# Optimization experiments

Hardware: AMD Instinct MI355X
Metric: run time of the kernel (lower is better)

## Reference

```python
import jax, jax.numpy as jnp
import numpy as np

N = 50000
F_IN = 256
HID = 64
HEADS = 4
NUM_CLASSES = 40
E = 1600000
NEG_SLOPE = 0.2
BN_EPS = 1e-5


def setup_inputs() -> dict:
    key = jax.random.key(0)
    ks = jax.random.split(key, 16)
    x = jax.random.normal(ks[0], (N, F_IN), dtype=jnp.float32)
    edge_index = jax.random.randint(ks[1], (2, E), 0, N, dtype=jnp.int64)
    # layer 1: GATConv(F_IN -> HID, heads=HEADS), PyG param layout
    W1 = jax.random.normal(ks[2], (F_IN, HEADS * HID), dtype=jnp.float32) / np.sqrt(F_IN)
    att_src1 = jax.random.normal(ks[3], (HEADS, HID), dtype=jnp.float32) / np.sqrt(HID)
    att_dst1 = jax.random.normal(ks[4], (HEADS, HID), dtype=jnp.float32) / np.sqrt(HID)
    bias1 = jnp.zeros((HEADS * HID,), dtype=jnp.float32)
    # BatchNorm1d(HEADS*HID), eval mode running stats
    gamma1 = jax.random.normal(ks[5], (HEADS * HID,), dtype=jnp.float32) * 0.1 + 1.0
    beta1 = jax.random.normal(ks[6], (HEADS * HID,), dtype=jnp.float32) * 0.1
    mean1 = jax.random.normal(ks[7], (HEADS * HID,), dtype=jnp.float32) * 0.1
    var1 = jax.random.uniform(ks[8], (HEADS * HID,), dtype=jnp.float32) + 0.5
    # layer 2: GATConv(HEADS*HID -> NUM_CLASSES, heads=1)
    W2 = jax.random.normal(ks[9], (HEADS * HID, NUM_CLASSES), dtype=jnp.float32) / np.sqrt(HEADS * HID)
    att_src2 = jax.random.normal(ks[10], (1, NUM_CLASSES), dtype=jnp.float32) / np.sqrt(NUM_CLASSES)
    att_dst2 = jax.random.normal(ks[11], (1, NUM_CLASSES), dtype=jnp.float32) / np.sqrt(NUM_CLASSES)
    bias2 = jnp.zeros((NUM_CLASSES,), dtype=jnp.float32)
    return {
        "x": x, "edge_index": edge_index,
        "W1": W1, "att_src1": att_src1, "att_dst1": att_dst1, "bias1": bias1,
        "gamma1": gamma1, "beta1": beta1, "mean1": mean1, "var1": var1,
        "W2": W2, "att_src2": att_src2, "att_dst2": att_dst2, "bias2": bias2,
    }


def gat_conv(x, src, dst, W, att_src, att_dst, bias, heads, out_ch):
    n = x.shape[0]
    h = (x @ W).reshape(n, heads, out_ch)          # [N, H, C]
    a_src = jnp.sum(h * att_src, axis=-1)           # [N, H]
    a_dst = jnp.sum(h * att_dst, axis=-1)           # [N, H]
    e = jax.nn.leaky_relu(a_src[src] + a_dst[dst], NEG_SLOPE)  # [E, H]
    # softmax over incoming edges per destination node
    e_max = jax.ops.segment_max(e, dst, num_segments=n)        # [N, H]
    e = jnp.exp(e - e_max[dst])
    denom = jax.ops.segment_sum(e, dst, num_segments=n)        # [N, H]
    alpha = e / (denom[dst] + 1e-16)                # [E, H]
    msg = h[src] * alpha[:, :, None]                # [E, H, C]
    out = jax.ops.segment_sum(msg, dst, num_segments=n)        # [N, H, C]
    return out.reshape(n, heads * out_ch) + bias


def reference(x, edge_index, W1, att_src1, att_dst1, bias1,
              gamma1, beta1, mean1, var1,
              W2, att_src2, att_dst2, bias2):
    # add self loops (PyG GATConv default add_self_loops=True)
    loop = jnp.arange(N, dtype=edge_index.dtype)
    src = jnp.concatenate([edge_index[0], loop])
    dst = jnp.concatenate([edge_index[1], loop])
    h = gat_conv(x, src, dst, W1, att_src1, att_dst1, bias1, HEADS, HID)
    # BatchNorm1d eval mode + ELU (dropout inactive in eval)
    h = (h - mean1) * jax.lax.rsqrt(var1 + BN_EPS) * gamma1 + beta1
    h = jax.nn.elu(h)
    out = gat_conv(h, src, dst, W2, att_src2, att_dst2, bias2, 1, NUM_CLASSES)
    return out
```

## Files before the change

kernel.cpp:

```cpp
#include <hip/hip_runtime.h>
#include <hip/hip_bf16.h>

#define NN 50000
#define FIN 256
#define F1 256
#define HEADS 4
#define HID 64
#define NC 40
#define NE 1600000
#define SLOPE 0.2f
#define LOG2E 1.44269504f
#define CHUNK 128
#define NB2 98
#define BSH 9
#define BCAP2 18000
#define TILE 2048
#define NBIN 782
#define NG1 782
#define G1PAD 40

typedef unsigned int u32;
typedef unsigned short u16;
typedef unsigned char u8;
typedef __attribute__((ext_vector_type(8))) short bf16x8;
typedef __attribute__((ext_vector_type(4))) float f32x4;

__device__ __forceinline__ float us2f(u32 u){ u32 b = u << 16; return __uint_as_float(b); }
__device__ __forceinline__ u16 f2bf(float f){
  u32 b = __float_as_uint(f);
  u32 r = (b + 0x7fffu + ((b >> 16) & 1u)) >> 16;
  return (u16)r;
}

__global__ __launch_bounds__(256) void k_prep(const int* __restrict__ ei,
      int* __restrict__ cnt, u32* __restrict__ bin,
      const float* __restrict__ W1, u16* __restrict__ w1h, u16* __restrict__ w1l,
      const float* __restrict__ W2, u16* __restrict__ w2h, u16* __restrict__ w2l){
  __shared__ int hcnt[NB2], hoff[NB2], gbase[NB2], hcur[NB2];
  __shared__ u32 staged[TILE];
  __shared__ u8  sbk[TILE];
  __shared__ int ci;
  int bid = blockIdx.x, tid = threadIdx.x;
  if(bid < NBIN){
    int e0 = bid * TILE;
    int nn = min(TILE, NE - e0);
    if(tid==0) ci = 0;
    for(int b=tid;b<NB2;b+=256) hcnt[b] = 0;
    __syncthreads();
    if(ei[2*(e0+tid)+1] != 0) atomicAdd(&ci, 1);
    __syncthreads();
    int i64 = (ci == 0);
    u32 val[TILE/256]; int bk[TILE/256];
    #pragma unroll
    for(int j=0;j<TILE/256;j++){
      int t = tid + j*256;
      if(t < nn){
        int i = e0 + t;
        int src = i64 ? ei[2*i] : ei[i];
        int dst = i64 ? ei[2*(NE+i)] : ei[NE+i];
        bk[j] = dst >> BSH;
        val[j] = (u32)src | ((u32)(dst & 511) << 16);
        atomicAdd(&hcnt[bk[j]], 1);
      } else bk[j] = -1;
    }
    __syncthreads();
    if(tid == 0){
      int run = 0;
      for(int b=0;b<NB2;b++){ hoff[b] = run; hcur[b] = run; run += hcnt[b]; }
    }
    __syncthreads();
    if(tid < NB2 && hcnt[tid] > 0) gbase[tid] = atomicAdd(&cnt[tid], hcnt[tid]);
    __syncthreads();
    #pragma unroll
    for(int j=0;j<TILE/256;j++){
      if(bk[j] >= 0){
        int pos = atomicAdd(&hcur[bk[j]], 1);
        staged[pos] = val[j];
        sbk[pos] = (u8)bk[j];
      }
    }
    __syncthreads();
    for(int s=tid; s<nn; s+=256){
      int b = sbk[s];
      int local = gbase[b] + (s - hoff[b]);
      if(local < BCAP2) bin[(size_t)b*BCAP2 + local] = staged[s];
    }
  } else if(bid < NBIN+256){
    int id = (bid-NBIN)*256 + tid;
    int n = id & 255, k = id >> 8;
    float v = W1[k*F1 + n];
    u16 h = f2bf(v);
    w1h[n*FIN + k] = h;
    w1l[n*FIN + k] = f2bf(v - us2f(h));
  } else {
    int id = (bid-(NBIN+256))*256 + tid;
    int col = id >> 8, k = id & 255;
    float v = (col < NC) ? W2[k*NC + col] : 0.f;
    u16 h = f2bf(v);
    w2h[col*F1 + k] = h;
    w2l[col*F1 + k] = f2bf(v - us2f(h));
  }
}

__global__ __launch_bounds__(256) void k_g1h(const float* __restrict__ x,
                                             const short* __restrict__ wh, const short* __restrict__ wl,
                                             const float* __restrict__ as1, const float* __restrict__ ad1,
                                             u16* __restrict__ h1b,
                                             float* __restrict__ aS, float* __restrict__ aD,
                                             const int* __restrict__ cnt, const u32* __restrict__ bin,
                                             int* __restrict__ rloc, int* __restrict__ bsum){
  __shared__ char smem[4*128*G1PAD*2];
  int tid = threadIdx.x;
  if(blockIdx.x >= NG1){
    int* dl = (int*)smem; int* s1 = dl + 512; int* s2 = s1 + 512;
    int b = blockIdx.x - NG1;
    for(int i=tid;i<512;i+=256) dl[i] = 0;
    __syncthreads();
    int n = min(cnt[b], BCAP2);
    const u32* bp = bin + (size_t)b*BCAP2;
    for(int i=tid;i<n;i+=256) atomicAdd(&dl[(bp[i]>>16)&511], 1);
    __syncthreads();
    for(int i=tid;i<512;i+=256) s1[i] = dl[i];
    __syncthreads();
    int* src = s1; int* dst = s2;
    for(int off=1; off<512; off<<=1){
      for(int i=tid;i<512;i+=256) dst[i] = src[i] + (i>=off ? src[i-off] : 0);
      __syncthreads();
      int* t = src; src = dst; dst = t;
    }
    for(int i=tid;i<512;i+=256) rloc[b*512+i] = src[i] - dl[i];
    if(tid==0) bsum[b] = src[511];
    return;
  }
  u16* Ah = (u16*)smem;
  u16* Al = Ah + 128*G1PAD;
  u16* Bh = Al + 128*G1PAD;
  u16* Bl = Bh + 128*G1PAD;
  int w = tid >> 6, lane = tid & 63;
  int lo = lane & 15, hi = lane >> 4;
  int bidm = blockIdx.x >> 1, bidn = blockIdx.x & 1;
  int rowbase = bidm*128, colbase = bidn*128;
  int wr = w >> 1, wc = w & 1;
  int r0 = tid >> 2, ch = tid & 3;
  int arow0 = rowbase + r0;      if(arow0 >= NN) arow0 = NN-1;
  int arow1 = rowbase + r0 + 64; if(arow1 >= NN) arow1 = NN-1;
  const float* pX0 = x + (size_t)arow0*FIN + ch*8;
  const float* pX1 = x + (size_t)arow1*FIN + ch*8;
  const short* pB0h = wh + (size_t)(colbase + r0)*FIN + ch*8;
  const short* pB1h = wh + (size_t)(colbase + r0 + 64)*FIN + ch*8;
  const short* pB0l = wl + (size_t)(colbase + r0)*FIN + ch*8;
  const short* pB1l = wl + (size_t)(colbase + r0 + 64)*FIN + ch*8;
  int so0 = r0*G1PAD + ch*8, so1 = (r0+64)*G1PAD + ch*8;
  f32x4 acc[4][4];
  #pragma unroll
  for(int rg=0;rg<4;rg++)
    #pragma unroll
    for(int tt=0;tt<4;tt++) acc[rg][tt] = (f32x4){0.f,0.f,0.f,0.f};
  for(int k0=0; k0<FIN; k0+=32){
    float4 xa0 = *(const float4*)(pX0 + k0);
    float4 xa1 = *(const float4*)(pX0 + k0 + 4);
    float4 xb0 = *(const float4*)(pX1 + k0);
    float4 xb1 = *(const float4*)(pX1 + k0 + 4);
    bf16x8 vb0 = *(const bf16x8*)(pB0h + k0);
    bf16x8 vb1 = *(const bf16x8*)(pB1h + k0);
    bf16x8 vb2 = *(const bf16x8*)(pB0l + k0);
    bf16x8 vb3 = *(const bf16x8*)(pB1l + k0);
    float v0[8] = {xa0.x,xa0.y,xa0.z,xa0.w,xa1.x,xa1.y,xa1.z,xa1.w};
    float v1[8] = {xb0.x,xb0.y,xb0.z,xb0.w,xb1.x,xb1.y,xb1.z,xb1.w};
    bf16x8 a0h, a0l, a1h, a1l;
    #pragma unroll
    for(int j=0;j<8;j++){
      u32 u = __float_as_uint(v0[j]);
      a0h[j] = (short)(u >> 16);
      float hf = __uint_as_float(u & 0xffff0000u);
      a0l[j] = (short)(__float_as_uint(v0[j] - hf) >> 16);
      u32 u2 = __float_as_uint(v1[j]);
      a1h[j] = (short)(u2 >> 16);
      float hf2 = __uint_as_float(u2 & 0xffff0000u);
      a1l[j] = (short)(__float_as_uint(v1[j] - hf2) >> 16);
    }
    __syncthreads();
    *(bf16x8*)&Ah[so0] = a0h; *(bf16x8*)&Ah[so1] = a1h;
    *(bf16x8*)&Al[so0] = a0l; *(bf16x8*)&Al[so1] = a1l;
    *(bf16x8*)&Bh[so0] = vb0; *(bf16x8*)&Bh[so1] = vb1;
    *(bf16x8*)&Bl[so0] = vb2; *(bf16x8*)&Bl[so1] = vb3;
    __syncthreads();
    bf16x8 ah[4], al[4];
    #pragma unroll
    for(int rg=0;rg<4;rg++){
      int ar = wr*64 + rg*16 + lo;
      ah[rg] = *(const bf16x8*)&Ah[ar*G1PAD + hi*8];
      al[rg] = *(const bf16x8*)&Al[ar*G1PAD + hi*8];
    }
    #pragma unroll
    for(int tt=0;tt<4;tt++){
      int bc = wc*64 + tt*16 + lo;
      bf16x8 bh = *(const bf16x8*)&Bh[bc*G1PAD + hi*8];
      bf16x8 bl = *(const bf16x8*)&Bl[bc*G1PAD + hi*8];
      #pragma unroll
      for(int rg=0;rg<4;rg++){
        acc[rg][tt] = __builtin_amdgcn_mfma_f32_16x16x32_bf16(ah[rg], bh, acc[rg][tt], 0, 0, 0);
        acc[rg][tt] = __builtin_amdgcn_mfma_f32_16x16x32_bf16(al[rg], bh, acc[rg][tt], 0, 0, 0);
        acc[rg][tt] = __builtin_amdgcn_mfma_f32_16x16x32_bf16(ah[rg], bl, acc[rg][tt], 0, 0, 0);
      }
    }
  }
  #pragma unroll
  for(int rg=0;rg<4;rg++){
    #pragma unroll
    for(int tt=0;tt<4;tt++){
      #pragma unroll
      for(int r=0;r<4;r++){
        int row = rowbase + wr*64 + rg*16 + hi*4 + r;
        if(row < NN) h1b[(size_t)row*F1 + colbase + wc*64 + tt*16 + lo] = f2bf(acc[rg][tt][r]);
      }
    }
  }
  int head = bidn*2 + wc;
  float ps[4][4], pd[4][4];
  #pragma unroll
  for(int rg=0;rg<4;rg++)
    #pragma unroll
    for(int r=0;r<4;r++){ ps[rg][r]=0.f; pd[rg][r]=0.f; }
  #pragma unroll
  for(int tt=0;tt<4;tt++){
    int col = colbase + wc*64 + tt*16 + lo;
    float sv = as1[col]*LOG2E, dv = ad1[col]*LOG2E;
    #pragma unroll
    for(int rg=0;rg<4;rg++)
      #pragma unroll
      for(int r=0;r<4;r++){ ps[rg][r] += acc[rg][tt][r]*sv; pd[rg][r] += acc[rg][tt][r]*dv; }
  }
  #pragma unroll
  for(int off=1; off<16; off<<=1){
    #pragma unroll
    for(int rg=0;rg<4;rg++)
      #pragma unroll
      for(int r=0;r<4;r++){
        ps[rg][r] += __shfl_xor(ps[rg][r], off, 64);
        pd[rg][r] += __shfl_xor(pd[rg][r], off, 64);
      }
  }
  if(lo == 0){
    #pragma unroll
    for(int rg=0;rg<4;rg++)
      #pragma unroll
      for(int r=0;r<4;r++){
        int row = rowbase + wr*64 + rg*16 + hi*4 + r;
        if(row < NN){ aS[row*HEADS+head] = ps[rg][r]; aD[row*HEADS+head] = pd[rg][r]; }
      }
  }
}

__global__ __launch_bounds__(256) void k_fill2(const int* __restrict__ cnt, const u32* __restrict__ bin,
                                               const int* __restrict__ rloc, const int* __restrict__ bsum,
                                               int* __restrict__ rowptr, int* __restrict__ adj){
  __shared__ int cur[512];
  __shared__ int sb[NB2];
  __shared__ int base_s;
  int b = blockIdx.x, tid = threadIdx.x;
  if(tid < NB2) sb[tid] = bsum[tid];
  __syncthreads();
  if(tid == 0){
    int run = 0;
    for(int i=0;i<b;i++) run += sb[i];
    base_s = run;
    if(b == NB2-1) rowptr[NN] = run + sb[b];
  }
  __syncthreads();
  int base = base_s;
  for(int i=tid;i<512;i+=256){
    int d = b*512 + i;
    int v = base + rloc[b*512+i];
    cur[i] = v;
    if(d < NN) rowptr[d] = v;
  }
  __syncthreads();
  int n = min(cnt[b], BCAP2);
  const u32* bp = bin + (size_t)b*BCAP2;
  for(int i=tid;i<n;i+=256){
    u32 v = bp[i];
    int p = atomicAdd(&cur[(v>>16)&511], 1);
    adj[p] = (int)(v & 0xffffu);
  }
}

__global__ __launch_bounds__(256) void k_agg1(const u16* __restrict__ h1b,
  const float* __restrict__ aS, const float* __restrict__ aD,
  const int* __restrict__ rowptr, const int* __restrict__ adj,
  const float* __restrict__ b1, const float* __restrict__ g1, const float* __restrict__ be1,
  const float* __restrict__ mn1, const float* __restrict__ vr1,
  float* __restrict__ h2){
  __shared__ float lw[4][CHUNK*4];
  __shared__ int   lsrc[4][CHUNK];
  int w = threadIdx.x >> 6, lane = threadIdx.x & 63;
  int node = blockIdx.x*4 + w;
  int g = lane >> 5, li = lane & 31;
  int hb = li >> 3;
  int beg = rowptr[node], end = rowptr[node+1];
  float4 ad4 = *(const float4*)&aD[node*HEADS];
  float den[4] = {0.f,0.f,0.f,0.f};
  float acc[8] = {0.f,0.f,0.f,0.f,0.f,0.f,0.f,0.f};
  int total = end - beg + 1;
  for(int c0=0; c0<total; c0+=CHUNK){
    int n = min(CHUNK, total - c0);
    for(int i=lane; i<n; i+=64){
      int e = beg + c0 + i;
      int src = (e < end) ? adj[e] : node;
      float4 s4 = *(const float4*)&aS[src*HEADS];
      float w0 = s4.x + ad4.x; w0 = w0>0.f?w0:SLOPE*w0; w0 = exp2f(fminf(w0,110.f));
      float w1 = s4.y + ad4.y; w1 = w1>0.f?w1:SLOPE*w1; w1 = exp2f(fminf(w1,110.f));
      float w2 = s4.z + ad4.z; w2 = w2>0.f?w2:SLOPE*w2; w2 = exp2f(fminf(w2,110.f));
      float w3 = s4.w + ad4.w; w3 = w3>0.f?w3:SLOPE*w3; w3 = exp2f(fminf(w3,110.f));
      lsrc[w][i] = src;
      *(float4*)&lw[w][i*4] = make_float4(w0,w1,w2,w3);
      den[0]+=w0; den[1]+=w1; den[2]+=w2; den[3]+=w3;
    }
    asm volatile("s_waitcnt lgkmcnt(0)" ::: "memory");
    #pragma unroll 2
    for(int i=0; i<n; i+=2){
      int e = i + g;
      bool ok = e < n;
      int src = ok ? lsrc[w][e] : node;
      float wg = ok ? lw[w][e*4 + hb] : 0.f;
      uint4 pv = *(const uint4*)&h1b[(size_t)src*F1 + li*8];
      acc[0] += wg*__uint_as_float(pv.x << 16);  acc[1] += wg*__uint_as_float(pv.x & 0xffff0000u);
      acc[2] += wg*__uint_as_float(pv.y << 16);  acc[3] += wg*__uint_as_float(pv.y & 0xffff0000u);
      acc[4] += wg*__uint_as_float(pv.z << 16);  acc[5] += wg*__uint_as_float(pv.z & 0xffff0000u);
      acc[6] += wg*__uint_as_float(pv.w << 16);  acc[7] += wg*__uint_as_float(pv.w & 0xffff0000u);
    }
  }
  #pragma unroll
  for(int off=1; off<64; off<<=1){
    #pragma unroll
    for(int q=0;q<4;q++) den[q] += __shfl_xor(den[q], off, 64);
  }
  #pragma unroll
  for(int k=0;k<8;k++) acc[k] += __shfl_xor(acc[k], 32, 64);
  if(lane < 32){
    float dsel = hb==0 ? den[0] : (hb==1 ? den[1] : (hb==2 ? den[2] : den[3]));
    float inv = 1.f/(dsel + 1e-16f);
    int c = li*8;
    float o[8];
    #pragma unroll
    for(int j=0;j<8;j++){
      float v = acc[j]*inv + b1[c+j];
      v = (v - mn1[c+j]) * rsqrtf(vr1[c+j] + 1e-5f) * g1[c+j] + be1[c+j];
      o[j] = v > 0.f ? v : (__expf(v) - 1.f);
    }
    *(float4*)&h2[(size_t)node*F1 + c]     = make_float4(o[0],o[1],o[2],o[3]);
    *(float4*)&h2[(size_t)node*F1 + c + 4] = make_float4(o[4],o[5],o[6],o[7]);
  }
}

__global__ __launch_bounds__(256) void k_gemm2(const float* __restrict__ h2,
    const short* __restrict__ w2h, const short* __restrict__ w2l,
    const float* __restrict__ as2, const float* __restrict__ ad2,
    u16* __restrict__ h2p, float* __restrict__ aS2, float* __restrict__ aD2){
  int w = threadIdx.x >> 6, lane = threadIdx.x & 63;
  int lo = lane & 15, hi = lane >> 4;
  int rowbase = blockIdx.x*64 + w*16;
  int arow = rowbase + lo; if(arow >= NN) arow = NN-1;
  f32x4 acc[3];
  #pragma unroll
  for(int tt=0;tt<3;tt++) acc[tt] = (f32x4){0.f,0.f,0.f,0.f};
  const float* xp = h2 + (size_t)arow*F1 + 8*hi;
  const short* bph = w2h + (size_t)lo*F1 + 8*hi;
  const short* bpl = w2l + (size_t)lo*F1 + 8*hi;
  for(int k0=0; k0<F1; k0+=32){
    float4 va = *(const float4*)(xp + k0);
    float4 vb = *(const float4*)(xp + k0 + 4);
    float v[8] = {va.x,va.y,va.z,va.w,vb.x,vb.y,vb.z,vb.w};
    bf16x8 ah, al;
    #pragma unroll
    for(int j=0;j<8;j++){
      u32 u = __float_as_uint(v[j]);
      ah[j] = (short)(u >> 16);
      float hf = __uint_as_float(u & 0xffff0000u);
      al[j] = (short)(__float_as_uint(v[j] - hf) >> 16);
    }
    #pragma unroll
    for(int tt=0;tt<3;tt++){
      bf16x8 bh = *(const bf16x8*)(bph + (size_t)tt*16*F1 + k0);
      bf16x8 bl = *(const bf16x8*)(bpl + (size_t)tt*16*F1 + k0);
      acc[tt] = __builtin_amdgcn_mfma_f32_16x16x32_bf16(ah, bh, acc[tt], 0, 0, 0);
      acc[tt] = __builtin_amdgcn_mfma_f32_16x16x32_bf16(al, bh, acc[tt], 0, 0, 0);
      acc[tt] = __builtin_amdgcn_mfma_f32_16x16x32_bf16(ah, bl, acc[tt], 0, 0, 0);
    }
  }
  float ps[4] = {0.f,0.f,0.f,0.f}, pd[4] = {0.f,0.f,0.f,0.f};
  #pragma unroll
  for(int tt=0;tt<3;tt++){
    int col = tt*16 + lo;
    float sv = (col < NC) ? as2[col]*LOG2E : 0.f;
    float dv = (col < NC) ? ad2[col]*LOG2E : 0.f;
    #pragma unroll
    for(int r=0;r<4;r++){
      int row = rowbase + hi*4 + r;
      if(row < NN && col < NC) h2p[(size_t)row*NC + col] = f2bf(acc[tt][r]);
      ps[r] += acc[tt][r]*sv; pd[r] += acc[tt][r]*dv;
    }
  }
  #pragma unroll
  for(int off=1; off<16; off<<=1){
    #pragma unroll
    for(int r=0;r<4;r++){ ps[r] += __shfl_xor(ps[r], off, 64); pd[r] += __shfl_xor(pd[r], off, 64); }
  }
  if(lo == 0){
    #pragma unroll
    for(int r=0;r<4;r++){
      int row = rowbase + hi*4 + r;
      if(row < NN){ aS2[row] = ps[r]; aD2[row] = pd[r]; }
    }
  }
}

__global__ __launch_bounds__(256) void k_agg2(const u16* __restrict__ h2p,
  const float* __restrict__ aS2, const float* __restrict__ aD2,
  const int* __restrict__ rowptr, const int* __restrict__ adj,
  const float* __restrict__ b2, float* __restrict__ out){
  __shared__ float lw[4][CHUNK];
  __shared__ int   lsrc[4][CHUNK];
  int w = threadIdx.x >> 6, lane = threadIdx.x & 63;
  int node = blockIdx.x*4 + w;
  int beg = rowptr[node], end = rowptr[node+1];
  float adv = aD2[node];
  float den = 0.f, acc = 0.f;
  int total = end - beg + 1;
  for(int c0=0; c0<total; c0+=CHUNK){
    int n = min(CHUNK, total - c0);
    for(int i=lane; i<n; i+=64){
      int e = beg + c0 + i;
      int src = (e < end) ? adj[e] : node;
      float ev = aS2[src] + adv; ev = ev>0.f?ev:SLOPE*ev;
      float wg = exp2f(fminf(ev,110.f));
      lsrc[w][i] = src;
      lw[w][i] = wg;
      den += wg;
    }
    asm volatile("s_waitcnt lgkmcnt(0)" ::: "memory");
    #pragma unroll 2
    for(int i=0;i<n;i++){
      int s = lsrc[w][i];
      float wg = lw[w][i];
      if(lane < NC) acc += wg * us2f(h2p[(size_t)s*NC + lane]);
    }
  }
  #pragma unroll
  for(int off=1; off<64; off<<=1) den += __shfl_xor(den, off, 64);
  if(lane < NC) out[(size_t)node*NC + lane] = acc/(den + 1e-16f) + b2[lane];
}

extern "C" void kernel_launch(void* const* d_in, const int* in_sizes, int n_in,
                              void* d_out, int out_size, void* d_ws, size_t ws_size,
                              hipStream_t stream){
  (void)in_sizes; (void)n_in; (void)out_size; (void)ws_size;
  const float* x   = (const float*)d_in[0];
  const int*   ei  = (const int*)d_in[1];
  const float* W1  = (const float*)d_in[2];
  const float* as1 = (const float*)d_in[3];
  const float* ad1 = (const float*)d_in[4];
  const float* b1  = (const float*)d_in[5];
  const float* g1  = (const float*)d_in[6];
  const float* be1 = (const float*)d_in[7];
  const float* mn1 = (const float*)d_in[8];
  const float* vr1 = (const float*)d_in[9];
  const float* W2  = (const float*)d_in[10];
  const float* as2 = (const float*)d_in[11];
  const float* ad2 = (const float*)d_in[12];
  const float* b2  = (const float*)d_in[13];

  char* ws = (char*)d_ws;
  u16*  h1b    = (u16*) (ws + 0);
  float* h2    = (float*)(ws + 25600000);
  u16*  h2p    = (u16*) (ws + 76800000);
  u16*  w1h    = (u16*) (ws + 76800000);
  u16*  w1l    = (u16*) (ws + 76931072);
  float* aS1   = (float*)(ws + 84800000);
  float* aD1   = (float*)(ws + 85600000);
  float* aS2   = (float*)(ws + 86400000);
  float* aD2   = (float*)(ws + 86600000);
  int*  rowptr = (int*)  (ws + 86800000);
  int*  adj    = (int*)  (ws + 87200016);
  u32*  bin    = (u32*)  (ws + 93700000);
  int*  cnt    = (int*)  (ws + 100800000);
  int*  rloc   = (int*)  (ws + 100801024);
  int*  bsum   = (int*)  (ws + 101002240);
  u16*  w2h    = (u16*)  (ws + 101003712);
  u16*  w2l    = (u16*)  (ws + 101028288);

  hipMemsetAsync(cnt, 0, NB2*sizeof(int), stream);
  k_prep  <<<NBIN+256+48, 256, 0, stream>>>(ei, cnt, bin, W1, w1h, w1l, W2, w2h, w2l);
  k_g1h   <<<NG1 + NB2, 256, 0, stream>>>(x, (const short*)w1h, (const short*)w1l,
                                          as1, ad1, h1b, aS1, aD1,
                                          cnt, bin, rloc, bsum);
  k_fill2 <<<NB2, 256, 0, stream>>>(cnt, bin, rloc, bsum, rowptr, adj);
  k_agg1  <<<NN/4, 256, 0, stream>>>(h1b, aS1, aD1, rowptr, adj, b1, g1, be1, mn1, vr1, h2);
  k_gemm2 <<<(NN+63)/64, 256, 0, stream>>>(h2, (const short*)w2h, (const short*)w2l,
                                           as2, ad2, h2p, aS2, aD2);
  k_agg2  <<<NN/4, 256, 0, stream>>>(h2p, aS2, aD2, rowptr, adj, b2, (float*)d_out);
}
```

Measured before the change: 339.5 us.

## Fold CSR fill into g1h bucket blocks using padded per-bucket adjacency

```diff
diff --git a/kernel.cpp b/kernel.cpp
--- a/kernel.cpp
+++ b/kernel.cpp
@@ -108,12 +108,14 @@
                                              u16* __restrict__ h1b,
                                              float* __restrict__ aS, float* __restrict__ aD,
                                              const int* __restrict__ cnt, const u32* __restrict__ bin,
-                                             int* __restrict__ rloc, int* __restrict__ bsum){
+                                             int* __restrict__ rowptr, int* __restrict__ rend,
+                                             int* __restrict__ adj){
   __shared__ char smem[4*128*G1PAD*2];
   int tid = threadIdx.x;
   if(blockIdx.x >= NG1){
     int* dl = (int*)smem; int* s1 = dl + 512; int* s2 = s1 + 512;
     int b = blockIdx.x - NG1;
+    int base = b * BCAP2;
     for(int i=tid;i<512;i+=256) dl[i] = 0;
     __syncthreads();
     int n = min(cnt[b], BCAP2);
@@ -128,8 +130,18 @@
       __syncthreads();
       int* t = src; src = dst; dst = t;
     }
-    for(int i=tid;i<512;i+=256) rloc[b*512+i] = src[i] - dl[i];
-    if(tid==0) bsum[b] = src[511];
+    for(int i=tid;i<512;i+=256){
+      int d = b*512 + i;
+      int excl = src[i] - dl[i];
+      if(d < NN){ rowptr[d] = base + excl; rend[d] = base + src[i]; }
+      dl[i] = base + excl;
+    }
+    __syncthreads();
+    for(int i=tid;i<n;i+=256){
+      u32 v = bp[i];
+      int p = atomicAdd(&dl[(v>>16)&511], 1);
+      adj[p] = (int)(v & 0xffffu);
+    }
     return;
   }
   u16* Ah = (u16*)smem;
@@ -252,42 +264,9 @@
   }
 }
 
-__global__ __launch_bounds__(256) void k_fill2(const int* __restrict__ cnt, const u32* __restrict__ bin,
-                                               const int* __restrict__ rloc, const int* __restrict__ bsum,
-                                               int* __restrict__ rowptr, int* __restrict__ adj){
-  __shared__ int cur[512];
-  __shared__ int sb[NB2];
-  __shared__ int base_s;
-  int b = blockIdx.x, tid = threadIdx.x;
-  if(tid < NB2) sb[tid] = bsum[tid];
-  __syncthreads();
-  if(tid == 0){
-    int run = 0;
-    for(int i=0;i<b;i++) run += sb[i];
-    base_s = run;
-    if(b == NB2-1) rowptr[NN] = run + sb[b];
-  }
-  __syncthreads();
-  int base = base_s;
-  for(int i=tid;i<512;i+=256){
-    int d = b*512 + i;
-    int v = base + rloc[b*512+i];
-    cur[i] = v;
-    if(d < NN) rowptr[d] = v;
-  }
-  __syncthreads();
-  int n = min(cnt[b], BCAP2);
-  const u32* bp = bin + (size_t)b*BCAP2;
-  for(int i=tid;i<n;i+=256){
-    u32 v = bp[i];
-    int p = atomicAdd(&cur[(v>>16)&511], 1);
-    adj[p] = (int)(v & 0xffffu);
-  }
-}
-
 __global__ __launch_bounds__(256) void k_agg1(const u16* __restrict__ h1b,
   const float* __restrict__ aS, const float* __restrict__ aD,
-  const int* __restrict__ rowptr, const int* __restrict__ adj,
+  const int* __restrict__ rowptr, const int* __restrict__ rend, const int* __restrict__ adj,
   const float* __restrict__ b1, const float* __restrict__ g1, const float* __restrict__ be1,
   const float* __restrict__ mn1, const float* __restrict__ vr1,
   float* __restrict__ h2){
@@ -297,7 +276,7 @@
   int node = blockIdx.x*4 + w;
   int g = lane >> 5, li = lane & 31;
   int hb = li >> 3;
-  int beg = rowptr[node], end = rowptr[node+1];
+  int beg = rowptr[node], end = rend[node];
   float4 ad4 = *(const float4*)&aD[node*HEADS];
   float den[4] = {0.f,0.f,0.f,0.f};
   float acc[8] = {0.f,0.f,0.f,0.f,0.f,0.f,0.f,0.f};
@@ -417,13 +396,13 @@
 
 __global__ __launch_bounds__(256) void k_agg2(const u16* __restrict__ h2p,
   const float* __restrict__ aS2, const float* __restrict__ aD2,
-  const int* __restrict__ rowptr, const int* __restrict__ adj,
+  const int* __restrict__ rowptr, const int* __restrict__ rend, const int* __restrict__ adj,
   const float* __restrict__ b2, float* __restrict__ out){
   __shared__ float lw[4][CHUNK];
   __shared__ int   lsrc[4][CHUNK];
   int w = threadIdx.x >> 6, lane = threadIdx.x & 63;
   int node = blockIdx.x*4 + w;
-  int beg = rowptr[node], end = rowptr[node+1];
+  int beg = rowptr[node], end = rend[node];
   float adv = aD2[node];
   float den = 0.f, acc = 0.f;
   int total = end - beg + 1;
@@ -481,22 +460,20 @@
   float* aS2   = (float*)(ws + 86400000);
   float* aD2   = (float*)(ws + 86600000);
   int*  rowptr = (int*)  (ws + 86800000);
+  int*  rend   = (int*)  (ws + 87000016);
   int*  adj    = (int*)  (ws + 87200016);
-  u32*  bin    = (u32*)  (ws + 93700000);
-  int*  cnt    = (int*)  (ws + 100800000);
-  int*  rloc   = (int*)  (ws + 100801024);
-  int*  bsum   = (int*)  (ws + 101002240);
-  u16*  w2h    = (u16*)  (ws + 101003712);
-  u16*  w2l    = (u16*)  (ws + 101028288);
+  u32*  bin    = (u32*)  (ws + 94300000);
+  int*  cnt    = (int*)  (ws + 101356000);
+  u16*  w2h    = (u16*)  (ws + 101357000);
+  u16*  w2l    = (u16*)  (ws + 101382000);
 
   hipMemsetAsync(cnt, 0, NB2*sizeof(int), stream);
   k_prep  <<<NBIN+256+48, 256, 0, stream>>>(ei, cnt, bin, W1, w1h, w1l, W2, w2h, w2l);
   k_g1h   <<<NG1 + NB2, 256, 0, stream>>>(x, (const short*)w1h, (const short*)w1l,
                                           as1, ad1, h1b, aS1, aD1,
-                                          cnt, bin, rloc, bsum);
-  k_fill2 <<<NB2, 256, 0, stream>>>(cnt, bin, rloc, bsum, rowptr, adj);
-  k_agg1  <<<NN/4, 256, 0, stream>>>(h1b, aS1, aD1, rowptr, adj, b1, g1, be1, mn1, vr1, h2);
+                                          cnt, bin, rowptr, rend, adj);
+  k_agg1  <<<NN/4, 256, 0, stream>>>(h1b, aS1, aD1, rowptr, rend, adj, b1, g1, be1, mn1, vr1, h2);
   k_gemm2 <<<(NN+63)/64, 256, 0, stream>>>(h2, (const short*)w2h, (const short*)w2l,
                                            as2, ad2, h2p, aS2, aD2);
-  k_agg2  <<<NN/4, 256, 0, stream>>>(h2p, aS2, aD2, rowptr, adj, b2, (float*)d_out);
-}
+  k_agg2  <<<NN/4, 256, 0, stream>>>(h2p, aS2, aD2, rowptr, rend, adj, b2, (float*)d_out);
+}
```

Result: no change. 338.1 us (-0.4%).
